# Optimization experiments

Hardware: AMD Instinct MI355X
Metric: run time of the kernel (lower is better)

Reference implementation:

```python
import jax, jax.numpy as jnp
import numpy as np

K = 20          # neighbors, default of knn/get_graph_feature
EPS = 1e-5      # BatchNorm eps (torch default)


def knn_idx(x, k):
    # x: [B,3,N] -> indices of k nearest neighbors [B,N,k]
    xx = jnp.sum(x * x, axis=1)                      # [B,N]
    inner = jnp.einsum('bdn,bdm->bnm', x, x)         # [B,N,N]
    neg_dist = 2.0 * inner - xx[:, :, None] - xx[:, None, :]  # -||xi-xj||^2
    return jax.lax.top_k(neg_dist, k)[1]             # largest == nearest


def graph_feature(x, k):
    # x: [B,D,N] -> [B,2D,N,k]  (channels = [neighbor feats, center feats])
    idx = knn_idx(x, k)                              # [B,N,k]
    xt = jnp.transpose(x, (0, 2, 1))                 # [B,N,D]
    nbr = jax.vmap(lambda p, i: p[i])(xt, idx)       # [B,N,k,D] gather
    ctr = jnp.broadcast_to(xt[:, :, None, :], nbr.shape)
    feat = jnp.concatenate([nbr, ctr], axis=3)       # [B,N,k,2D]
    return jnp.transpose(feat, (0, 3, 1, 2))         # [B,2D,N,k]


def conv1x1(y, W):
    # Conv2d(kernel_size=1, bias=False): y [B,C,N,k], W [O,C]
    return jnp.einsum('bcnk,oc->bonk', y, W)


def bn_relu(y, g, b):
    # BatchNorm2d in training mode (batch statistics over B,N,k per channel)
    m = jnp.mean(y, axis=(0, 2, 3), keepdims=True)
    v = jnp.mean((y - m) ** 2, axis=(0, 2, 3), keepdims=True)
    yn = (y - m) * jax.lax.rsqrt(v + EPS)
    return jax.nn.relu(yn * g[None, :, None, None] + b[None, :, None, None])


def setup_inputs() -> dict:
    key = jax.random.key(0)
    ks = jax.random.split(key, 20)
    B, D, N = 8, 3, 2048
    x = jax.random.normal(ks[0], (B, D, N), dtype=jnp.float32)
    def w(k, o, c):
        return jax.random.normal(k, (o, c), dtype=jnp.float32) * (1.0 / np.sqrt(c))
    inp = {
        'x': x,
        'W1': w(ks[1], 64, 6),   'W2': w(ks[2], 64, 64),
        'W3': w(ks[3], 128, 64), 'W4': w(ks[4], 256, 128),
        'W5': w(ks[5], 512, 512),
    }
    for i, c in zip(range(1, 6), (64, 64, 128, 256, 512)):
        inp[f'g{i}'] = 1.0 + 0.1 * jax.random.normal(ks[5 + i], (c,), dtype=jnp.float32)
        inp[f'b{i}'] = 0.1 * jax.random.normal(ks[10 + i], (c,), dtype=jnp.float32)
    return inp


def reference(x, W1, W2, W3, W4, W5, g1, b1, g2, b2, g3, b3, g4, b4, g5, b5):
    # DGCNN core: single kNN graph feature + 4 EdgeConv 1x1 convs with
    # per-layer max over neighbors, concat, final 1x1 conv, pad to 1024 ch.
    f = graph_feature(x, K)                          # [B,6,N,K]
    h1 = bn_relu(conv1x1(f, W1), g1, b1)             # [B,64,N,K]
    x1 = jnp.max(h1, axis=-1, keepdims=True)
    h2 = bn_relu(conv1x1(h1, W2), g2, b2)            # [B,64,N,K]
    x2 = jnp.max(h2, axis=-1, keepdims=True)
    h3 = bn_relu(conv1x1(h2, W3), g3, b3)            # [B,128,N,K]
    x3 = jnp.max(h3, axis=-1, keepdims=True)
    h4 = bn_relu(conv1x1(h3, W4), g4, b4)            # [B,256,N,K]
    x4 = jnp.max(h4, axis=-1, keepdims=True)
    cat = jnp.concatenate([x1, x2, x3, x4], axis=1)  # [B,512,N,1]
    h5 = bn_relu(conv1x1(cat, W5), g5, b5)[..., 0]   # [B,512,N]
    out = jnp.pad(h5, ((0, 0), (0, 1024 - 512), (0, 0)))  # pad channels -> 1024
    return out.astype(jnp.float32)
```

## Files before the change

### kernel.cpp

```cpp
#include <hip/hip_runtime.h>

#define BB  8
#define NP  2048
#define KNB 20
#define KP  10
#define SS  40960

typedef unsigned short bf16_t;
typedef __attribute__((ext_vector_type(8))) short short8_t;
typedef __attribute__((ext_vector_type(4))) float f32x4;

static __device__ __forceinline__ float bf2f(unsigned short u) {
    return __uint_as_float(((unsigned)u) << 16);
}
static __device__ __forceinline__ bf16_t f2bf(float f) {
    unsigned u = __float_as_uint(f);
    return (bf16_t)((u + 0x7fffu + ((u >> 16) & 1u)) >> 16);
}

#if __has_builtin(__builtin_amdgcn_fmed3f)
#define MED3(a, b, c) __builtin_amdgcn_fmed3f((a), (b), (c))
#else
#define MED3(a, b, c) fmaxf(fminf((a), (b)), fminf(fmaxf((a), (b)), (c)))
#endif

static __device__ __forceinline__ float negdist(float4 me, float4 p) {
    float d = me.x * p.x + me.y * p.y + me.z * p.z;
    return 2.0f * d - me.w - p.w;
}

#define BDECL(t) float bv##t = -3.4e38f;
#define MCH(t, p) bv##t = MED3(v, bv##p, bv##t);
#define BSHIFT(t, n) bv##t = bv##n;
#define FDECL(t) float fv##t = -3.4e38f;
#define FMCH(t, p) fv##t = MED3(v, fv##p, fv##t);
#define FSHIFT(t, n) fv##t = fv##n;

__global__ __launch_bounds__(256) void knn_kernel(const float* __restrict__ x,
                                                  int* __restrict__ idx) {
    __shared__ float4 tile[2064];
    __shared__ int   cnt[16];
    __shared__ float svv[16][44];
    __shared__ int   svj[16][44];
    const int tid  = threadIdx.x;
    const int b    = blockIdx.x >> 7;
    const int pblk = blockIdx.x & 127;
    const int pl   = tid >> 4;
    const int seg  = tid & 15;
    const int i    = pblk * 16 + pl;
    const float* xb = x + (size_t)b * 3 * NP;

    for (int j = tid; j < NP; j += 256) {
        float a0 = xb[j], a1 = xb[NP + j], a2 = xb[2 * NP + j];
        tile[j + (j >> 7)] = make_float4(a0, a1, a2, a0 * a0 + a1 * a1 + a2 * a2);
    }
    if (tid < 16) cnt[tid] = 0;
    __syncthreads();
    const float4 me = tile[i + (i >> 7)];
    const float4* tseg = &tile[seg * 129];

    BDECL(0) BDECL(1) BDECL(2) BDECL(3) BDECL(4)
    BDECL(5) BDECL(6) BDECL(7) BDECL(8) BDECL(9)
    for (int t = 0; t < 128; ++t) {
        float v = negdist(me, tseg[t]);
        MCH(9,8) MCH(8,7) MCH(7,6) MCH(6,5) MCH(5,4)
        MCH(4,3) MCH(3,2) MCH(2,1) MCH(1,0)
        bv0 = fmaxf(bv0, v);
    }

    float theta = -3.4e38f;
    int pops = 0;
    for (int r = 0; r < KNB; ++r) {
        float mv = bv0; int ms = seg;
#pragma unroll
        for (int s = 1; s <= 8; s <<= 1) {
            float ov = __shfl_xor(mv, s, 64);
            int   os = __shfl_xor(ms, s, 64);
            if (ov > mv || (ov == mv && os < ms)) { mv = ov; ms = os; }
        }
        if (seg == ms) {
            BSHIFT(0,1) BSHIFT(1,2) BSHIFT(2,3) BSHIFT(3,4) BSHIFT(4,5)
            BSHIFT(5,6) BSHIFT(6,7) BSHIFT(7,8) BSHIFT(8,9)
            bv9 = -3.4e38f;
            ++pops;
        }
        theta = mv;
    }

    int bad = (pops >= KP) ? 1 : 0;
#pragma unroll
    for (int s = 1; s <= 8; s <<= 1) bad |= __shfl_xor(bad, s, 64);
    if (bad) {
        FDECL(0)  FDECL(1)  FDECL(2)  FDECL(3)  FDECL(4)
        FDECL(5)  FDECL(6)  FDECL(7)  FDECL(8)  FDECL(9)
        FDECL(10) FDECL(11) FDECL(12) FDECL(13) FDECL(14)
        FDECL(15) FDECL(16) FDECL(17) FDECL(18) FDECL(19)
        for (int t = 0; t < 128; ++t) {
            float v = negdist(me, tseg[t]);
            FMCH(19,18) FMCH(18,17) FMCH(17,16) FMCH(16,15) FMCH(15,14)
            FMCH(14,13) FMCH(13,12) FMCH(12,11) FMCH(11,10) FMCH(10,9)
            FMCH(9,8)   FMCH(8,7)   FMCH(7,6)   FMCH(6,5)   FMCH(5,4)
            FMCH(4,3)   FMCH(3,2)   FMCH(2,1)   FMCH(1,0)
            fv0 = fmaxf(fv0, v);
        }
        theta = -3.4e38f;
        for (int r = 0; r < KNB; ++r) {
            float mv = fv0; int ms = seg;
#pragma unroll
            for (int s = 1; s <= 8; s <<= 1) {
                float ov = __shfl_xor(mv, s, 64);
                int   os = __shfl_xor(ms, s, 64);
                if (ov > mv || (ov == mv && os < ms)) { mv = ov; ms = os; }
            }
            if (seg == ms) {
                FSHIFT(0,1)   FSHIFT(1,2)   FSHIFT(2,3)   FSHIFT(3,4)   FSHIFT(4,5)
                FSHIFT(5,6)   FSHIFT(6,7)   FSHIFT(7,8)   FSHIFT(8,9)   FSHIFT(9,10)
                FSHIFT(10,11) FSHIFT(11,12) FSHIFT(12,13) FSHIFT(13,14) FSHIFT(14,15)
                FSHIFT(15,16) FSHIFT(16,17) FSHIFT(17,18) FSHIFT(18,19)
                fv19 = -3.4e38f;
            }
            theta = mv;
        }
    }

    for (int t = 0; t < 128; ++t) {
        float v = negdist(me, tseg[t]);
        if (v >= theta) {
            int k = atomicAdd(&cnt[pl], 1);
            if (k < 44) { svv[pl][k] = v; svj[pl][k] = seg * 128 + t; }
        }
    }
    __syncthreads();

    int n = cnt[pl]; if (n > 44) n = 44;
    int* o = idx + ((size_t)b * NP + i) * KNB;
    for (int e = seg; e < n; e += 16) {
        float v = svv[pl][e]; int j = svj[pl][e];
        int rank = 0;
        for (int q = 0; q < n; ++q) {
            float vq = svv[pl][q]; int jq = svj[pl][q];
            rank += (vq > v || (vq == v && jq < j)) ? 1 : 0;
        }
        if (rank < KNB) o[rank] = j;
    }
}

__global__ void gather_kernel(const float* __restrict__ x, const int* __restrict__ idx,
                              bf16_t* __restrict__ f) {
    int s = blockIdx.x * 256 + threadIdx.x;
    int b = blockIdx.y;
    int n = s / KNB;
    int j = idx[(size_t)b * SS + s];
    const float* xb = x + (size_t)b * 3 * NP;
    ushort4 u0, u1;
    u0.x = f2bf(xb[j]);          u0.y = f2bf(xb[NP + j]);
    u0.z = f2bf(xb[2 * NP + j]); u0.w = f2bf(xb[n]);
    u1.x = f2bf(xb[NP + n]);     u1.y = f2bf(xb[2 * NP + n]);
    u1.z = 0; u1.w = 0;
    ushort4 z4; z4.x = 0; z4.y = 0; z4.z = 0; z4.w = 0;
    bf16_t* fb = f + ((size_t)b * SS + s) * 32;
    *(ushort4*)(fb)      = u0;
    *(ushort4*)(fb + 4)  = u1;
    *(ushort4*)(fb + 8)  = z4;
    *(ushort4*)(fb + 12) = z4;
    *(ushort4*)(fb + 16) = z4;
    *(ushort4*)(fb + 20) = z4;
    *(ushort4*)(fb + 24) = z4;
    *(ushort4*)(fb + 28) = z4;
}

__global__ void wconv_kernel(const float* __restrict__ src, bf16_t* __restrict__ dst,
                             int O, int CI, int CIP) {
    int t = blockIdx.x * 256 + threadIdx.x;
    if (t >= O * CIP) return;
    int o = t / CIP, cp = t - o * CIP;
    dst[t] = (cp < CI) ? f2bf(src[o * CI + cp]) : (bf16_t)0;
}

__global__ void zstats_kernel(float* __restrict__ p) {
    p[blockIdx.x * 256 + threadIdx.x] = 0.f;
}

__global__ void bnrelu_kernel(bf16_t* __restrict__ y, const float* __restrict__ ab,
                              int C) {
    size_t e0 = ((size_t)blockIdx.x * 256 + threadIdx.x) * 8;
    int c0 = (int)(e0 & (size_t)(C - 1));
    uint4 r = *(uint4*)(y + e0);
    float4 a0 = *(const float4*)(ab + c0);
    float4 a1 = *(const float4*)(ab + c0 + 4);
    float4 d0 = *(const float4*)(ab + C + c0);
    float4 d1 = *(const float4*)(ab + C + c0 + 4);
    float v0 = bf2f((unsigned short)(r.x & 0xffffu)), v1 = bf2f((unsigned short)(r.x >> 16));
    float v2 = bf2f((unsigned short)(r.y & 0xffffu)), v3 = bf2f((unsigned short)(r.y >> 16));
    float v4 = bf2f((unsigned short)(r.z & 0xffffu)), v5 = bf2f((unsigned short)(r.z >> 16));
    float v6 = bf2f((unsigned short)(r.w & 0xffffu)), v7 = bf2f((unsigned short)(r.w >> 16));
    v0 = fmaxf(fmaf(a0.x, v0, d0.x), 0.f); v1 = fmaxf(fmaf(a0.y, v1, d0.y), 0.f);
    v2 = fmaxf(fmaf(a0.z, v2, d0.z), 0.f); v3 = fmaxf(fmaf(a0.w, v3, d0.w), 0.f);
    v4 = fmaxf(fmaf(a1.x, v4, d1.x), 0.f); v5 = fmaxf(fmaf(a1.y, v5, d1.y), 0.f);
    v6 = fmaxf(fmaf(a1.z, v6, d1.z), 0.f); v7 = fmaxf(fmaf(a1.w, v7, d1.w), 0.f);
    r.x = (unsigned)f2bf(v0) | ((unsigned)f2bf(v1) << 16);
    r.y = (unsigned)f2bf(v2) | ((unsigned)f2bf(v3) << 16);
    r.z = (unsigned)f2bf(v4) | ((unsigned)f2bf(v5) << 16);
    r.w = (unsigned)f2bf(v6) | ((unsigned)f2bf(v7) << 16);
    *(uint4*)(y + e0) = r;
}

#define MF(A, B, C) C = __builtin_amdgcn_mfma_f32_16x16x32_bf16(A, B, C, 0, 0, 0);

#define LGKM_BARRIER() { \
    asm volatile("s_waitcnt lgkmcnt(0)" ::: "memory"); \
    __builtin_amdgcn_s_barrier(); \
    asm volatile("" ::: "memory"); }

#define TILE1(CC, CT, STt, YT) { \
    ushort4 t4; \
    t4.x = f2bf(CC[0]); t4.y = f2bf(CC[1]); \
    t4.z = f2bf(CC[2]); t4.w = f2bf(CC[3]); \
    *(ushort4*)&YT[w * 32 + (STt) * 16 + col][(CT) * 16 + quad * 4] = t4; }

#define EPILOGUE(ITV) { \
    bf16_t (*yt)[68] = ytile[(ITV) & (NBUF - 1)]; \
    TILE1(c00,0,0,yt) TILE1(c10,1,0,yt) TILE1(c20,2,0,yt) TILE1(c30,3,0,yt) \
    TILE1(c01,0,1,yt) TILE1(c11,1,1,yt) TILE1(c21,2,1,yt) TILE1(c31,3,1,yt) \
    LGKM_BARRIER() \
    if constexpr (ST) { \
        const int row0 = blockIdx.x * (SR * NS) + (ITV) * SR; \
        for (int i = tid; i < SR * 16; i += NW * 64) { \
            int row = i >> 4, c4 = (i & 15) * 4; \
            ushort4 yv = *(const ushort4*)&yt[row][c4]; \
            *(ushort4*)(Yout + ((size_t)b * SROWS + row0 + row) * COUT_T + cob + c4) = yv; \
            if constexpr (!POOL) { \
                float v0 = bf2f(yv.x), v1 = bf2f(yv.y); \
                float v2 = bf2f(yv.z), v3 = bf2f(yv.w); \
                sv0 += v0; qv0 = fmaf(v0, v0, qv0); \
                sv1 += v1; qv1 = fmaf(v1, v1, qv1); \
                sv2 += v2; qv2 = fmaf(v2, v2, qv2); \
                sv3 += v3; qv3 = fmaf(v3, v3, qv3); \
            } \
        } \
    } \
    if constexpr (POOL) { \
        const int nbase = (blockIdx.x * NS + (ITV)) * 8; \
        for (int i = tid; i < 8 * 32; i += NW * 64) { \
            const int nl = i >> 5, c2 = (i & 31) * 2; \
            float m0 = -3.4e38f, m1 = -3.4e38f; \
            _Pragma("unroll") \
            for (int k = 0; k < KNB; ++k) { \
                unsigned u = *(const unsigned*)&yt[nl * 20 + k][c2]; \
                float v0 = bf2f((unsigned short)(u & 0xffffu)); \
                float v1 = bf2f((unsigned short)(u >> 16)); \
                m0 = fmaxf(m0, v0); m1 = fmaxf(m1, v1); \
                svA += v0; qvA = fmaf(v0, v0, qvA); \
                svB += v1; qvB = fmaf(v1, v1, qvB); \
            } \
            unsigned r2 = (unsigned)f2bf(m0) | ((unsigned)f2bf(m1) << 16); \
            *(unsigned*)(poolOut + ((size_t)b * NP + nbase + nl) * 512 + chofs + cob + c2) = r2; \
        } \
    } \
}

template<int CIN, int COUT_T, int SROWS, int NW, int NS, bool POOL, bool ST, bool PRE>
__global__ __launch_bounds__(320)
void mconv(const bf16_t* __restrict__ H, const bf16_t* __restrict__ Wb,
           bf16_t* __restrict__ Yout, bf16_t* __restrict__ poolOut,
           int chofs, float* __restrict__ stats) {
    constexpr int SR = NW * 32;
    constexpr int NKK = CIN / 32;
    constexpr int NBUF = (NS > 1) ? 2 : 1;
    __shared__ bf16_t ytile[NBUF][SR][68];
    __shared__ float redS[NW][64];
    __shared__ float redQ[NW][64];
    const int tid  = threadIdx.x;
    const int lane = tid & 63, col = lane & 15, quad = lane >> 4, q8 = quad * 8;
    const int w    = tid >> 6;
    const int cob  = blockIdx.y * 64;
    const int b    = blockIdx.z;
    const bf16_t* wp = Wb + (size_t)(cob + col) * CIN + q8;

    float svA = 0.f, svB = 0.f, qvA = 0.f, qvB = 0.f;
    float sv0 = 0.f, sv1 = 0.f, sv2 = 0.f, sv3 = 0.f;
    float qv0 = 0.f, qv1 = 0.f, qv2 = 0.f, qv3 = 0.f;

    if constexpr (PRE) {
        short8_t Af0[NKK], Af1[NKK], Af2[NKK], Af3[NKK];
#pragma unroll
        for (int kk = 0; kk < NKK; ++kk) {
            Af0[kk] = *(const short8_t*)(wp + kk * 32);
            Af1[kk] = *(const short8_t*)(wp + 16 * CIN + kk * 32);
            Af2[kk] = *(const short8_t*)(wp + 32 * CIN + kk * 32);
            Af3[kk] = *(const short8_t*)(wp + 48 * CIN + kk * 32);
        }

        short8_t cb0[NKK], cb1[NKK], nb0[NKK], nb1[NKK];
        {
            const int sb = blockIdx.x * (SR * NS) + w * 32;
            const bf16_t* hp0 = H + ((size_t)b * SROWS + sb + col) * CIN + q8;
            const bf16_t* hp1 = hp0 + 16 * CIN;
#pragma unroll
            for (int kk = 0; kk < NKK; ++kk) {
                cb0[kk] = *(const short8_t*)(hp0 + kk * 32);
                cb1[kk] = *(const short8_t*)(hp1 + kk * 32);
            }
        }

#pragma unroll 1
        for (int it = 0; it < NS; ++it) {
            if (it + 1 < NS) {
                const int sb = blockIdx.x * (SR * NS) + (it + 1) * SR + w * 32;
                const bf16_t* hp0 = H + ((size_t)b * SROWS + sb + col) * CIN + q8;
                const bf16_t* hp1 = hp0 + 16 * CIN;
#pragma unroll
                for (int kk = 0; kk < NKK; ++kk) {
                    nb0[kk] = *(const short8_t*)(hp0 + kk * 32);
                    nb1[kk] = *(const short8_t*)(hp1 + kk * 32);
                }
            }

            f32x4 c00 = {0.f,0.f,0.f,0.f}, c10 = c00, c20 = c00, c30 = c00;
            f32x4 c01 = c00, c11 = c00, c21 = c00, c31 = c00;
#pragma unroll
            for (int kk = 0; kk < NKK; ++kk) {
                MF(Af0[kk], cb0[kk], c00) MF(Af1[kk], cb0[kk], c10)
                MF(Af2[kk], cb0[kk], c20) MF(Af3[kk], cb0[kk], c30)
                MF(Af0[kk], cb1[kk], c01) MF(Af1[kk], cb1[kk], c11)
                MF(Af2[kk], cb1[kk], c21) MF(Af3[kk], cb1[kk], c31)
            }

            EPILOGUE(it)

            if (it + 1 < NS) {
#pragma unroll
                for (int kk = 0; kk < NKK; ++kk) { cb0[kk] = nb0[kk]; cb1[kk] = nb1[kk]; }
            }
        }
    } else {
        for (int it = 0; it < NS; ++it) {
            const int sb = blockIdx.x * (SR * NS) + it * SR + w * 32;
            const bf16_t* hp0 = H + ((size_t)b * SROWS + sb + col) * CIN + q8;
            const bf16_t* hp1 = hp0 + 16 * CIN;

            f32x4 c00 = {0.f,0.f,0.f,0.f}, c10 = c00, c20 = c00, c30 = c00;
            f32x4 c01 = c00, c11 = c00, c21 = c00, c31 = c00;

            short8_t a0c = *(const short8_t*)(wp);
            short8_t a1c = *(const short8_t*)(wp + 16 * CIN);
            short8_t a2c = *(const short8_t*)(wp + 32 * CIN);
            short8_t a3c = *(const short8_t*)(wp + 48 * CIN);
            short8_t b0c = *(const short8_t*)(hp0);
            short8_t b1c = *(const short8_t*)(hp1);

#pragma unroll 1
            for (int k0 = 0; k0 < CIN; k0 += 32) {
                short8_t a0n, a1n, a2n, a3n, b0n, b1n;
                if (k0 + 32 < CIN) {
                    a0n = *(const short8_t*)(wp + k0 + 32);
                    a1n = *(const short8_t*)(wp + 16 * CIN + k0 + 32);
                    a2n = *(const short8_t*)(wp + 32 * CIN + k0 + 32);
                    a3n = *(const short8_t*)(wp + 48 * CIN + k0 + 32);
                    b0n = *(const short8_t*)(hp0 + k0 + 32);
                    b1n = *(const short8_t*)(hp1 + k0 + 32);
                }
                MF(a0c, b0c, c00) MF(a1c, b0c, c10) MF(a2c, b0c, c20) MF(a3c, b0c, c30)
                MF(a0c, b1c, c01) MF(a1c, b1c, c11) MF(a2c, b1c, c21) MF(a3c, b1c, c31)
                if (k0 + 32 < CIN) {
                    a0c = a0n; a1c = a1n; a2c = a2n; a3c = a3n;
                    b0c = b0n; b1c = b1n;
                }
            }

            EPILOGUE(it)
        }
    }

    if constexpr (POOL) {
        svA += __shfl_xor(svA, 32, 64); qvA += __shfl_xor(qvA, 32, 64);
        svB += __shfl_xor(svB, 32, 64); qvB += __shfl_xor(qvB, 32, 64);
        if (lane < 32) {
            const int c2 = lane * 2;
            redS[w][c2] = svA; redS[w][c2 + 1] = svB;
            redQ[w][c2] = qvA; redQ[w][c2 + 1] = qvB;
        }
    } else if constexpr (ST) {
        sv0 += __shfl_xor(sv0, 16, 64); qv0 += __shfl_xor(qv0, 16, 64);
        sv1 += __shfl_xor(sv1, 16, 64); qv1 += __shfl_xor(qv1, 16, 64);
        sv2 += __shfl_xor(sv2, 16, 64); qv2 += __shfl_xor(qv2, 16, 64);
        sv3 += __shfl_xor(sv3, 16, 64); qv3 += __shfl_xor(qv3, 16, 64);
        sv0 += __shfl_xor(sv0, 32, 64); qv0 += __shfl_xor(qv0, 32, 64);
        sv1 += __shfl_xor(sv1, 32, 64); qv1 += __shfl_xor(qv1, 32, 64);
        sv2 += __shfl_xor(sv2, 32, 64); qv2 += __shfl_xor(qv2, 32, 64);
        sv3 += __shfl_xor(sv3, 32, 64); qv3 += __shfl_xor(qv3, 32, 64);
        if (lane < 16) {
            const int c4 = lane * 4;
            redS[w][c4]     = sv0; redS[w][c4 + 1] = sv1;
            redS[w][c4 + 2] = sv2; redS[w][c4 + 3] = sv3;
            redQ[w][c4]     = qv0; redQ[w][c4 + 1] = qv1;
            redQ[w][c4 + 2] = qv2; redQ[w][c4 + 3] = qv3;
        }
    }
    __syncthreads();
    if (tid < 64) {
        float sv = 0.f, qv = 0.f;
#pragma unroll
        for (int ch = 0; ch < NW; ++ch) { sv += redS[ch][tid]; qv += redQ[ch][tid]; }
        atomicAdd(&stats[cob + tid], sv);
        atomicAdd(&stats[COUT_T + cob + tid], qv);
    }
}

__global__ void bn_finalize(const float* __restrict__ stats,
                            const float* __restrict__ g, const float* __restrict__ bt,
                            float* __restrict__ ab, int C, float invM) {
    int c = blockIdx.x * 64 + threadIdx.x;
    if (c >= C) return;
    float mean = stats[c] * invM;
    float var  = fmaxf(stats[C + c] * invM - mean * mean, 0.f);
    float a = g[c] * rsqrtf(var + 1e-5f);
    ab[c] = a;
    ab[C + c] = fmaf(-mean, a, bt[c]);
}

__global__ void pool_convert(const bf16_t* __restrict__ pr, const float* __restrict__ ab,
                             bf16_t* __restrict__ xc, int C, int chofs, int logC) {
    int t = blockIdx.x * 256 + threadIdx.x;
    int c = t & (C - 1);
    int rest = t >> logC;
    int n = rest & (NP - 1);
    int b = rest >> 11;
    size_t p = ((size_t)b * NP + n) * 512 + chofs + c;
    float v = bf2f(pr[p]);
    xc[p] = f2bf(fmaxf(fmaf(ab[c], v, ab[C + c]), 0.f));
}

__global__ __launch_bounds__(256) void out_kernel(const bf16_t* __restrict__ y5,
                                                  const float* __restrict__ ab,
                                                  float* __restrict__ out) {
    __shared__ float lds[32][512];
    const int t  = threadIdx.x;
    const int nb = blockIdx.x * 32;
    const int b  = blockIdx.y;
#pragma unroll
    for (int k = 0; k < 8; ++k) {
        int ch  = t + k * 256;
        int row = ch >> 6;
        int c8  = (ch & 63) * 8;
        const bf16_t* yp = y5 + ((size_t)b * NP + nb + row) * 512 + c8;
        ushort4 u0 = *(const ushort4*)(yp);
        ushort4 u1 = *(const ushort4*)(yp + 4);
        float4 a0 = *(const float4*)(ab + c8);
        float4 a1 = *(const float4*)(ab + c8 + 4);
        float4 d0 = *(const float4*)(ab + 512 + c8);
        float4 d1 = *(const float4*)(ab + 512 + c8 + 4);
        lds[row][c8 + 0] = fmaxf(fmaf(a0.x, bf2f(u0.x), d0.x), 0.f);
        lds[row][c8 + 1] = fmaxf(fmaf(a0.y, bf2f(u0.y), d0.y), 0.f);
        lds[row][c8 + 2] = fmaxf(fmaf(a0.z, bf2f(u0.z), d0.z), 0.f);
        lds[row][c8 + 3] = fmaxf(fmaf(a0.w, bf2f(u0.w), d0.w), 0.f);
        lds[row][c8 + 4] = fmaxf(fmaf(a1.x, bf2f(u1.x), d1.x), 0.f);
        lds[row][c8 + 5] = fmaxf(fmaf(a1.y, bf2f(u1.y), d1.y), 0.f);
        lds[row][c8 + 6] = fmaxf(fmaf(a1.z, bf2f(u1.z), d1.z), 0.f);
        lds[row][c8 + 7] = fmaxf(fmaf(a1.w, bf2f(u1.w), d1.w), 0.f);
    }
    __syncthreads();
    const int n4   = t & 7;
    const int crow = t >> 3;
#pragma unroll
    for (int cc = 0; cc < 16; ++cc) {
        int c = crow + cc * 32;
        float4 v;
        v.x = lds[n4 * 4 + 0][c];
        v.y = lds[n4 * 4 + 1][c];
        v.z = lds[n4 * 4 + 2][c];
        v.w = lds[n4 * 4 + 3][c];
        *(float4*)(out + ((size_t)b * 1024 + c) * NP + nb + n4 * 4) = v;
    }
}

__global__ void zout_kernel(float* __restrict__ out) {
    size_t idx4 = (size_t)blockIdx.x * 256 + threadIdx.x;
    size_t off  = idx4 * 4;
    size_t per_b = (size_t)512 * NP;
    size_t b = off / per_b;
    size_t r = off - b * per_b;
    float4 z = make_float4(0.f, 0.f, 0.f, 0.f);
    *(float4*)(out + (b * 1024 + 512) * NP + r) = z;
}

extern "C" void kernel_launch(void* const* d_in, const int* in_sizes, int n_in,
                              void* d_out, int out_size, void* d_ws, size_t ws_size,
                              hipStream_t stream) {
    (void)in_sizes; (void)n_in; (void)out_size; (void)ws_size;
    const float* x  = (const float*)d_in[0];
    const float* W1 = (const float*)d_in[1];
    const float* W2 = (const float*)d_in[2];
    const float* W3 = (const float*)d_in[3];
    const float* W4 = (const float*)d_in[4];
    const float* W5 = (const float*)d_in[5];
    const float* g1 = (const float*)d_in[6];  const float* b1 = (const float*)d_in[7];
    const float* g2 = (const float*)d_in[8];  const float* b2 = (const float*)d_in[9];
    const float* g3 = (const float*)d_in[10]; const float* b3 = (const float*)d_in[11];
    const float* g4 = (const float*)d_in[12]; const float* b4 = (const float*)d_in[13];
    const float* g5 = (const float*)d_in[14]; const float* b5 = (const float*)d_in[15];

    char* ws = (char*)d_ws;
    bf16_t* f    = (bf16_t*)(ws + 0);
    bf16_t* y2   = (bf16_t*)(ws + 0);
    bf16_t* y5   = (bf16_t*)(ws + 0);
    bf16_t* y1   = (bf16_t*)(ws + 41943040);
    bf16_t* y3   = (bf16_t*)(ws + 41943040);
    bf16_t* poolraw = (bf16_t*)(ws + 125829120);
    bf16_t* xcat    = (bf16_t*)(ws + 142606336);
    bf16_t* Wball   = (bf16_t*)(ws + 159383552);
    bf16_t* W1b = Wball;
    bf16_t* W2b = Wball + 2048;
    bf16_t* W3b = Wball + 6144;
    bf16_t* W4b = Wball + 14336;
    bf16_t* W5b = Wball + 47104;
    float* stats = (float*)(ws + 160002048);
    float* ab    = (float*)(ws + 160010240);
    int*  idx    = (int*)  (ws + 160018432);

    float* st1 = stats;        float* st2 = stats + 128;  float* st3 = stats + 256;
    float* st4 = stats + 512;  float* st5 = stats + 1024;
    float* ab1 = ab;       float* ab2 = ab + 128;  float* ab3 = ab + 256;
    float* ab4 = ab + 512; float* ab5 = ab + 1024;
    const float invM14 = 1.f / (float)(BB * SS);
    const float invM5  = 1.f / (float)(BB * NP);

    zstats_kernel<<<8, 256, 0, stream>>>(stats);
    wconv_kernel<<<8,    256, 0, stream>>>(W1, W1b, 64, 6, 32);
    wconv_kernel<<<16,   256, 0, stream>>>(W2, W2b, 64, 64, 64);
    wconv_kernel<<<32,   256, 0, stream>>>(W3, W3b, 128, 64, 64);
    wconv_kernel<<<128,  256, 0, stream>>>(W4, W4b, 256, 128, 128);
    wconv_kernel<<<1024, 256, 0, stream>>>(W5, W5b, 512, 512, 512);

    knn_kernel<<<1024, 256, 0, stream>>>(x, idx);
    gather_kernel<<<dim3(160, BB), 256, 0, stream>>>(x, idx, f);

    zout_kernel<<<8192, 256, 0, stream>>>((float*)d_out);

    mconv<32, 64, SS, 5, 8, true, true, true><<<dim3(32, 1, BB), 320, 0, stream>>>(
        f, W1b, y1, poolraw, 0, st1);
    bn_finalize<<<1, 64, 0, stream>>>(st1, g1, b1, ab1, 64, invM14);
    pool_convert<<<4096, 256, 0, stream>>>(poolraw, ab1, xcat, 64, 0, 6);
    bnrelu_kernel<<<10240, 256, 0, stream>>>(y1, ab1, 64);

    mconv<64, 64, SS, 5, 8, true, true, true><<<dim3(32, 1, BB), 320, 0, stream>>>(
        y1, W2b, y2, poolraw, 64, st2);
    bn_finalize<<<1, 64, 0, stream>>>(st2, g2, b2, ab2, 64, invM14);
    pool_convert<<<4096, 256, 0, stream>>>(poolraw, ab2, xcat, 64, 64, 6);
    bnrelu_kernel<<<10240, 256, 0, stream>>>(y2, ab2, 64);

    mconv<64, 128, SS, 5, 8, true, true, true><<<dim3(32, 2, BB), 320, 0, stream>>>(
        y2, W3b, y3, poolraw, 128, st3);
    bn_finalize<<<2, 64, 0, stream>>>(st3, g3, b3, ab3, 128, invM14);
    pool_convert<<<8192, 256, 0, stream>>>(poolraw, ab3, xcat, 128, 128, 7);
    bnrelu_kernel<<<20480, 256, 0, stream>>>(y3, ab3, 128);

    mconv<128, 256, SS, 5, 16, true, false, true><<<dim3(16, 4, BB), 320, 0, stream>>>(
        y3, W4b, nullptr, poolraw, 256, st4);
    bn_finalize<<<4, 64, 0, stream>>>(st4, g4, b4, ab4, 256, invM14);
    pool_convert<<<16384, 256, 0, stream>>>(poolraw, ab4, xcat, 256, 256, 8);

    mconv<512, 512, NP, 4, 1, false, true, false><<<dim3(16, 8, BB), 256, 0, stream>>>(
        xcat, W5b, y5, nullptr, 0, st5);
    bn_finalize<<<8, 64, 0, stream>>>(st5, g5, b5, ab5, 512, invM5);

    out_kernel<<<dim3(64, BB), 256, 0, stream>>>(y5, ab5, (float*)d_out);
}
```

Measured before the change: 423.6 us.

## Process multiple 64-channel output groups per block to reuse activation fragments

Adds a template parameter G so each mconv block computes G groups of 64 output channels, reusing the loaded activation (B) fragments across groups while holding G sets of weights in registers. Layers 3 and 4 use G=2, which halves redundant activation reads from global memory; layer 4 also changes from 16 steps on a 16x4 grid to 8 steps on a 32x2 grid. Per-group BN statistics are reduced with extra barriers. The cost is higher register pressure from the doubled weight fragments, which could lower occupancy or cause spills, and less parallelism on layer 3 since its grid shrinks from 2 channel blocks to 1.

```diff
diff --git a/kernel.cpp b/kernel.cpp
--- a/kernel.cpp
+++ b/kernel.cpp
@@ -218,17 +218,18 @@
     t4.z = f2bf(CC[2]); t4.w = f2bf(CC[3]); \
     *(ushort4*)&YT[w * 32 + (STt) * 16 + col][(CT) * 16 + quad * 4] = t4; }
 
-#define EPILOGUE(ITV) { \
-    bf16_t (*yt)[68] = ytile[(ITV) & (NBUF - 1)]; \
+#define EPILOGUE(PH, GI) { \
+    bf16_t (*yt)[68] = ytile[(PH) & (NBUF - 1)]; \
+    const int cobg = cob + (GI) * 64; \
     TILE1(c00,0,0,yt) TILE1(c10,1,0,yt) TILE1(c20,2,0,yt) TILE1(c30,3,0,yt) \
     TILE1(c01,0,1,yt) TILE1(c11,1,1,yt) TILE1(c21,2,1,yt) TILE1(c31,3,1,yt) \
     LGKM_BARRIER() \
     if constexpr (ST) { \
-        const int row0 = blockIdx.x * (SR * NS) + (ITV) * SR; \
+        const int row0 = blockIdx.x * (SR * NS) + (ITV_OF(PH)) * SR; \
         for (int i = tid; i < SR * 16; i += NW * 64) { \
             int row = i >> 4, c4 = (i & 15) * 4; \
             ushort4 yv = *(const ushort4*)&yt[row][c4]; \
-            *(ushort4*)(Yout + ((size_t)b * SROWS + row0 + row) * COUT_T + cob + c4) = yv; \
+            *(ushort4*)(Yout + ((size_t)b * SROWS + row0 + row) * COUT_T + cobg + c4) = yv; \
             if constexpr (!POOL) { \
                 float v0 = bf2f(yv.x), v1 = bf2f(yv.y); \
                 float v2 = bf2f(yv.z), v3 = bf2f(yv.w); \
@@ -240,7 +241,7 @@
         } \
     } \
     if constexpr (POOL) { \
-        const int nbase = (blockIdx.x * NS + (ITV)) * 8; \
+        const int nbase = (blockIdx.x * NS + (ITV_OF(PH))) * 8; \
         for (int i = tid; i < 8 * 32; i += NW * 64) { \
             const int nl = i >> 5, c2 = (i & 31) * 2; \
             float m0 = -3.4e38f, m1 = -3.4e38f; \
@@ -250,45 +251,52 @@
                 float v0 = bf2f((unsigned short)(u & 0xffffu)); \
                 float v1 = bf2f((unsigned short)(u >> 16)); \
                 m0 = fmaxf(m0, v0); m1 = fmaxf(m1, v1); \
-                svA += v0; qvA = fmaf(v0, v0, qvA); \
-                svB += v1; qvB = fmaf(v1, v1, qvB); \
+                svA[GI] += v0; qvA[GI] = fmaf(v0, v0, qvA[GI]); \
+                svB[GI] += v1; qvB[GI] = fmaf(v1, v1, qvB[GI]); \
             } \
             unsigned r2 = (unsigned)f2bf(m0) | ((unsigned)f2bf(m1) << 16); \
-            *(unsigned*)(poolOut + ((size_t)b * NP + nbase + nl) * 512 + chofs + cob + c2) = r2; \
+            *(unsigned*)(poolOut + ((size_t)b * NP + nbase + nl) * 512 + chofs + cobg + c2) = r2; \
         } \
     } \
 }
 
-template<int CIN, int COUT_T, int SROWS, int NW, int NS, bool POOL, bool ST, bool PRE>
+#define ITV_OF(PH) ((PH) / G)
+
+template<int CIN, int COUT_T, int SROWS, int NW, int NS, int G, bool POOL, bool ST, bool PRE>
 __global__ __launch_bounds__(320)
 void mconv(const bf16_t* __restrict__ H, const bf16_t* __restrict__ Wb,
            bf16_t* __restrict__ Yout, bf16_t* __restrict__ poolOut,
            int chofs, float* __restrict__ stats) {
     constexpr int SR = NW * 32;
     constexpr int NKK = CIN / 32;
-    constexpr int NBUF = (NS > 1) ? 2 : 1;
+    constexpr int NBUF = (NS * G > 1) ? 2 : 1;
     __shared__ bf16_t ytile[NBUF][SR][68];
     __shared__ float redS[NW][64];
     __shared__ float redQ[NW][64];
     const int tid  = threadIdx.x;
     const int lane = tid & 63, col = lane & 15, quad = lane >> 4, q8 = quad * 8;
     const int w    = tid >> 6;
-    const int cob  = blockIdx.y * 64;
+    const int cob  = blockIdx.y * (64 * G);
     const int b    = blockIdx.z;
-    const bf16_t* wp = Wb + (size_t)(cob + col) * CIN + q8;
-
-    float svA = 0.f, svB = 0.f, qvA = 0.f, qvB = 0.f;
+
+    float svA[G], svB[G], qvA[G], qvB[G];
+#pragma unroll
+    for (int g = 0; g < G; ++g) { svA[g] = 0.f; svB[g] = 0.f; qvA[g] = 0.f; qvB[g] = 0.f; }
     float sv0 = 0.f, sv1 = 0.f, sv2 = 0.f, sv3 = 0.f;
     float qv0 = 0.f, qv1 = 0.f, qv2 = 0.f, qv3 = 0.f;
 
     if constexpr (PRE) {
-        short8_t Af0[NKK], Af1[NKK], Af2[NKK], Af3[NKK];
-#pragma unroll
-        for (int kk = 0; kk < NKK; ++kk) {
-            Af0[kk] = *(const short8_t*)(wp + kk * 32);
-            Af1[kk] = *(const short8_t*)(wp + 16 * CIN + kk * 32);
-            Af2[kk] = *(const short8_t*)(wp + 32 * CIN + kk * 32);
-            Af3[kk] = *(const short8_t*)(wp + 48 * CIN + kk * 32);
+        short8_t Af0[G][NKK], Af1[G][NKK], Af2[G][NKK], Af3[G][NKK];
+#pragma unroll
+        for (int g = 0; g < G; ++g) {
+            const bf16_t* wpg = Wb + (size_t)(cob + g * 64 + col) * CIN + q8;
+#pragma unroll
+            for (int kk = 0; kk < NKK; ++kk) {
+                Af0[g][kk] = *(const short8_t*)(wpg + kk * 32);
+                Af1[g][kk] = *(const short8_t*)(wpg + 16 * CIN + kk * 32);
+                Af2[g][kk] = *(const short8_t*)(wpg + 32 * CIN + kk * 32);
+                Af3[g][kk] = *(const short8_t*)(wpg + 48 * CIN + kk * 32);
+            }
         }
 
         short8_t cb0[NKK], cb1[NKK], nb0[NKK], nb1[NKK];
@@ -316,17 +324,19 @@
                 }
             }
 
-            f32x4 c00 = {0.f,0.f,0.f,0.f}, c10 = c00, c20 = c00, c30 = c00;
-            f32x4 c01 = c00, c11 = c00, c21 = c00, c31 = c00;
-#pragma unroll
-            for (int kk = 0; kk < NKK; ++kk) {
-                MF(Af0[kk], cb0[kk], c00) MF(Af1[kk], cb0[kk], c10)
-                MF(Af2[kk], cb0[kk], c20) MF(Af3[kk], cb0[kk], c30)
-                MF(Af0[kk], cb1[kk], c01) MF(Af1[kk], cb1[kk], c11)
-                MF(Af2[kk], cb1[kk], c21) MF(Af3[kk], cb1[kk], c31)
-            }
-
-            EPILOGUE(it)
+#pragma unroll
+            for (int g = 0; g < G; ++g) {
+                f32x4 c00 = {0.f,0.f,0.f,0.f}, c10 = c00, c20 = c00, c30 = c00;
+                f32x4 c01 = c00, c11 = c00, c21 = c00, c31 = c00;
+#pragma unroll
+                for (int kk = 0; kk < NKK; ++kk) {
+                    MF(Af0[g][kk], cb0[kk], c00) MF(Af1[g][kk], cb0[kk], c10)
+                    MF(Af2[g][kk], cb0[kk], c20) MF(Af3[g][kk], cb0[kk], c30)
+                    MF(Af0[g][kk], cb1[kk], c01) MF(Af1[g][kk], cb1[kk], c11)
+                    MF(Af2[g][kk], cb1[kk], c21) MF(Af3[g][kk], cb1[kk], c31)
+                }
+                EPILOGUE(it * G + g, g)
+            }
 
             if (it + 1 < NS) {
 #pragma unroll
@@ -336,6 +346,7 @@
     } else {
         for (int it = 0; it < NS; ++it) {
             const int sb = blockIdx.x * (SR * NS) + it * SR + w * 32;
+            const bf16_t* wp = Wb + (size_t)(cob + col) * CIN + q8;
             const bf16_t* hp0 = H + ((size_t)b * SROWS + sb + col) * CIN + q8;
             const bf16_t* hp1 = hp0 + 16 * CIN;
 
@@ -368,17 +379,31 @@
                 }
             }
 
-            EPILOGUE(it)
+            EPILOGUE(it, 0)
         }
     }
 
     if constexpr (POOL) {
-        svA += __shfl_xor(svA, 32, 64); qvA += __shfl_xor(qvA, 32, 64);
-        svB += __shfl_xor(svB, 32, 64); qvB += __shfl_xor(qvB, 32, 64);
-        if (lane < 32) {
-            const int c2 = lane * 2;
-            redS[w][c2] = svA; redS[w][c2 + 1] = svB;
-            redQ[w][c2] = qvA; redQ[w][c2 + 1] = qvB;
+#pragma unroll
+        for (int g = 0; g < G; ++g) {
+            float sA = svA[g] + __shfl_xor(svA[g], 32, 64);
+            float qA = qvA[g] + __shfl_xor(qvA[g], 32, 64);
+            float sB = svB[g] + __shfl_xor(svB[g], 32, 64);
+            float qB = qvB[g] + __shfl_xor(qvB[g], 32, 64);
+            if (lane < 32) {
+                const int c2 = lane * 2;
+                redS[w][c2] = sA; redS[w][c2 + 1] = sB;
+                redQ[w][c2] = qA; redQ[w][c2 + 1] = qB;
+            }
+            __syncthreads();
+            if (tid < 64) {
+                float sv = 0.f, qv = 0.f;
+#pragma unroll
+                for (int ch = 0; ch < NW; ++ch) { sv += redS[ch][tid]; qv += redQ[ch][tid]; }
+                atomicAdd(&stats[cob + g * 64 + tid], sv);
+                atomicAdd(&stats[COUT_T + cob + g * 64 + tid], qv);
+            }
+            if (g + 1 < G) __syncthreads();
         }
     } else if constexpr (ST) {
         sv0 += __shfl_xor(sv0, 16, 64); qv0 += __shfl_xor(qv0, 16, 64);
@@ -396,14 +421,14 @@
             redQ[w][c4]     = qv0; redQ[w][c4 + 1] = qv1;
             redQ[w][c4 + 2] = qv2; redQ[w][c4 + 3] = qv3;
         }
-    }
-    __syncthreads();
-    if (tid < 64) {
-        float sv = 0.f, qv = 0.f;
-#pragma unroll
-        for (int ch = 0; ch < NW; ++ch) { sv += redS[ch][tid]; qv += redQ[ch][tid]; }
-        atomicAdd(&stats[cob + tid], sv);
-        atomicAdd(&stats[COUT_T + cob + tid], qv);
+        __syncthreads();
+        if (tid < 64) {
+            float sv = 0.f, qv = 0.f;
+#pragma unroll
+            for (int ch = 0; ch < NW; ++ch) { sv += redS[ch][tid]; qv += redQ[ch][tid]; }
+            atomicAdd(&stats[cob + tid], sv);
+            atomicAdd(&stats[COUT_T + cob + tid], qv);
+        }
     }
 }
 
@@ -537,30 +562,30 @@
 
     zout_kernel<<<8192, 256, 0, stream>>>((float*)d_out);
 
-    mconv<32, 64, SS, 5, 8, true, true, true><<<dim3(32, 1, BB), 320, 0, stream>>>(
+    mconv<32, 64, SS, 5, 8, 1, true, true, true><<<dim3(32, 1, BB), 320, 0, stream>>>(
         f, W1b, y1, poolraw, 0, st1);
     bn_finalize<<<1, 64, 0, stream>>>(st1, g1, b1, ab1, 64, invM14);
     pool_convert<<<4096, 256, 0, stream>>>(poolraw, ab1, xcat, 64, 0, 6);
     bnrelu_kernel<<<10240, 256, 0, stream>>>(y1, ab1, 64);
 
-    mconv<64, 64, SS, 5, 8, true, true, true><<<dim3(32, 1, BB), 320, 0, stream>>>(
+    mconv<64, 64, SS, 5, 8, 1, true, true, true><<<dim3(32, 1, BB), 320, 0, stream>>>(
         y1, W2b, y2, poolraw, 64, st2);
     bn_finalize<<<1, 64, 0, stream>>>(st2, g2, b2, ab2, 64, invM14);
     pool_convert<<<4096, 256, 0, stream>>>(poolraw, ab2, xcat, 64, 64, 6);
     bnrelu_kernel<<<10240, 256, 0, stream>>>(y2, ab2, 64);
 
-    mconv<64, 128, SS, 5, 8, true, true, true><<<dim3(32, 2, BB), 320, 0, stream>>>(
+    mconv<64, 128, SS, 5, 8, 2, true, true, true><<<dim3(32, 1, BB), 320, 0, stream>>>(
         y2, W3b, y3, poolraw, 128, st3);
     bn_finalize<<<2, 64, 0, stream>>>(st3, g3, b3, ab3, 128, invM14);
     pool_convert<<<8192, 256, 0, stream>>>(poolraw, ab3, xcat, 128, 128, 7);
     bnrelu_kernel<<<20480, 256, 0, stream>>>(y3, ab3, 128);
 
-    mconv<128, 256, SS, 5, 16, true, false, true><<<dim3(16, 4, BB), 320, 0, stream>>>(
+    mconv<128, 256, SS, 5, 8, 2, true, false, true><<<dim3(32, 2, BB), 320, 0, stream>>>(
         y3, W4b, nullptr, poolraw, 256, st4);
     bn_finalize<<<4, 64, 0, stream>>>(st4, g4, b4, ab4, 256, invM14);
     pool_convert<<<16384, 256, 0, stream>>>(poolraw, ab4, xcat, 256, 256, 8);
 
-    mconv<512, 512, NP, 4, 1, false, true, false><<<dim3(16, 8, BB), 256, 0, stream>>>(
+    mconv<512, 512, NP, 4, 1, 1, false, true, false><<<dim3(16, 8, BB), 256, 0, stream>>>(
         xcat, W5b, y5, nullptr, 0, st5);
     bn_finalize<<<8, 64, 0, stream>>>(st5, g5, b5, ab5, 512, invM5);
 
```

New measurement: 437.4 us. +3.2%, slower.
